# Performance work log

Hardware: AMD Instinct MI355X
Metric: run time of the kernel (lower is better)

## Reference

```python
import jax, jax.numpy as jnp
import numpy as np

DIM, HEADS, DIM_HEAD = 1024, 16, 64
DIM_INNER = HEADS * DIM_HEAD  # 1024
SCALE = DIM_HEAD ** -0.5


def _rope(t):
    # t: [b, h, n, d]; interleaved-pair RoPE (lucidrains rotary-embedding-torch default)
    d = t.shape[-1]
    n = t.shape[-2]
    inv_freq = 1.0 / (10000.0 ** (jnp.arange(0, d, 2, dtype=jnp.float32) / d))
    angles = jnp.arange(n, dtype=jnp.float32)[:, None] * inv_freq[None, :]  # [n, d/2]
    cos, sin = jnp.cos(angles), jnp.sin(angles)
    t1, t2 = t[..., 0::2], t[..., 1::2]
    r1 = t1 * cos - t2 * sin
    r2 = t1 * sin + t2 * cos
    return jnp.stack([r1, r2], axis=-1).reshape(t.shape)


def setup_inputs() -> dict:
    key = jax.random.key(0)
    ks = jax.random.split(key, 8)
    b, n = 2, 2048
    inp = {
        "x": jax.random.normal(ks[0], (b, n, DIM), dtype=jnp.float32),
        "value_residual": jax.random.normal(ks[1], (b, HEADS, n, DIM_HEAD), dtype=jnp.float32),
        "gamma": jnp.ones((DIM,), dtype=jnp.float32),
        "w_qkv": jax.random.normal(ks[2], (DIM, 3 * DIM_INNER), dtype=jnp.float32) * (DIM ** -0.5),
        "w_mix": jax.random.normal(ks[3], (DIM, HEADS), dtype=jnp.float32) * (DIM ** -0.5),
        "b_mix": jnp.zeros((HEADS,), dtype=jnp.float32),
        "w_gates": jax.random.normal(ks[4], (DIM, HEADS), dtype=jnp.float32) * (DIM ** -0.5),
        "b_gates": jnp.zeros((HEADS,), dtype=jnp.float32),
        "w_out": jax.random.normal(ks[5], (DIM_INNER, DIM), dtype=jnp.float32) * (DIM_INNER ** -0.5),
    }
    return inp


def reference(x, value_residual, gamma, w_qkv, w_mix, b_mix, w_gates, b_gates, w_out):
    b, n, _ = x.shape
    # RMSNorm (lucidrains style: F.normalize * sqrt(dim) * gamma)
    norm = jnp.sqrt(jnp.sum(x * x, axis=-1, keepdims=True))
    xn = x / jnp.maximum(norm, 1e-12) * (DIM ** 0.5) * gamma

    qkv = xn @ w_qkv  # [b, n, 3*h*d]
    qkv = qkv.reshape(b, n, 3, HEADS, DIM_HEAD)
    q, k, v = [jnp.transpose(qkv[:, :, i], (0, 2, 1, 3)) for i in range(3)]  # [b,h,n,d]
    original_values = v

    # learned value-residual lerp
    mix = jax.nn.sigmoid(xn @ w_mix + b_mix)            # [b, n, h]
    mix = jnp.transpose(mix, (0, 2, 1))[..., None]       # [b, h, n, 1]
    v = v * (1.0 - mix) + value_residual * mix

    # rotary on q, k
    q = _rope(q)
    k = _rope(k)

    scores = jnp.einsum("bhid,bhjd->bhij", q, k) * SCALE
    attn = jax.nn.softmax(scores, axis=-1)
    out = jnp.einsum("bhij,bhjd->bhid", attn, v)         # [b, h, n, d]

    gates = jax.nn.sigmoid(xn @ w_gates + b_gates)       # [b, n, h]
    out = out * jnp.transpose(gates, (0, 2, 1))[..., None]

    out = jnp.transpose(out, (0, 2, 1, 3)).reshape(b, n, DIM_INNER)
    return out @ w_out, original_values
```

## Files before the change

kernel.cpp:

```cpp
#include <hip/hip_runtime.h>
#include <hip/hip_bf16.h>
#include <math.h>

#define DIMSZ 1024
#define HEADS 16
#define DHEAD 64
#define NSEQ  2048
#define BATCH 2
#define ROWS  (BATCH*NSEQ)
#define SCALE 0.125f
#define LOG2E 1.4426950408889634f

typedef __attribute__((ext_vector_type(8))) short short8;
typedef __attribute__((ext_vector_type(4))) float floatx4;

#define MFMA16(a,b,c) __builtin_amdgcn_mfma_f32_16x16x32_bf16(a,b,c,0,0,0)

__device__ __forceinline__ void gl2lds16(const void* g, void* l) {
    __builtin_amdgcn_global_load_lds(
        (const __attribute__((address_space(1))) unsigned int*)g,
        (__attribute__((address_space(3))) unsigned int*)l, 16, 0, 0);
}

__device__ __forceinline__ unsigned short bf16r(float a) {
    unsigned u = __float_as_uint(a);
    u += 0x7fff + ((u >> 16) & 1);
    return (unsigned short)(u >> 16);
}
__device__ __forceinline__ unsigned pack_bf16(float a, float b) {
    unsigned ua = __float_as_uint(a), ub = __float_as_uint(b);
    ua += 0x7fff + ((ua >> 16) & 1);
    ub += 0x7fff + ((ub >> 16) & 1);
    return (ua >> 16) | (ub & 0xffff0000u);
}
__device__ __forceinline__ float2 bf2f(unsigned u) {
    float2 r;
    r.x = __uint_as_float(u << 16);
    r.y = __uint_as_float(u & 0xffff0000u);
    return r;
}
__device__ __forceinline__ float fexp2(float x) {
#if __has_builtin(__builtin_amdgcn_exp2f)
    return __builtin_amdgcn_exp2f(x);
#else
    return exp2f(x);
#endif
}
__device__ __forceinline__ float fsin_rev(float x) {
#if __has_builtin(__builtin_amdgcn_sinf)
    return __builtin_amdgcn_sinf(x);
#else
    return __sinf(x * 6.28318530717958647692f);
#endif
}
__device__ __forceinline__ float fcos_rev(float x) {
#if __has_builtin(__builtin_amdgcn_cosf)
    return __builtin_amdgcn_cosf(x);
#else
    return __cosf(x * 6.28318530717958647692f);
#endif
}

__global__ __launch_bounds__(256) void transpose_all_kernel(
    const float* __restrict__ w_qkv, const float* __restrict__ w_out,
    const float* __restrict__ w_mix, const float* __restrict__ w_gates,
    unsigned short* __restrict__ wqkvT, unsigned short* __restrict__ woutT,
    unsigned short* __restrict__ wmgT)
{
    __shared__ float t[32][33];
    const int tx = threadIdx.x & 31, tyy = threadIdx.x >> 5;
    const int bx = blockIdx.x;
    const int k0 = blockIdx.y * 32;
    if (bx < 128) {
        const float* src;
        unsigned short* dst;
        int N, n0;
        if (bx < 96) { src = w_qkv; dst = wqkvT; N = 3*DIMSZ; n0 = bx*32; }
        else         { src = w_out; dst = woutT; N = DIMSZ;   n0 = (bx-96)*32; }
        #pragma unroll
        for (int i = 0; i < 4; i++)
            t[tyy*4 + i][tx] = src[(size_t)(k0 + tyy*4 + i)*N + n0 + tx];
        __syncthreads();
        #pragma unroll
        for (int i = 0; i < 4; i++)
            dst[(size_t)(n0 + tyy*4 + i)*DIMSZ + k0 + tx] = bf16r(t[tx][tyy*4 + i]);
    } else {
        #pragma unroll
        for (int i = 0; i < 4; i++) {
            const int kk = k0 + tyy*4 + i;
            t[tyy*4 + i][tx] = (tx < 16) ? w_mix[kk*16 + tx]
                                         : w_gates[kk*16 + (tx - 16)];
        }
        __syncthreads();
        #pragma unroll
        for (int i = 0; i < 4; i++)
            wmgT[(size_t)(tyy*4 + i)*DIMSZ + k0 + tx] = bf16r(t[tx][tyy*4 + i]);
    }
}

__global__ __launch_bounds__(256) void rmsnorm_kernel(
    const float* __restrict__ x, const float* __restrict__ gamma,
    unsigned short* __restrict__ xnb)
{
    const int row = blockIdx.x;
    const int tid = threadIdx.x;
    __shared__ float wred[4];

    const float4 xv = ((const float4*)(x + (size_t)row * DIMSZ))[tid];
    float ss = xv.x*xv.x + xv.y*xv.y + xv.z*xv.z + xv.w*xv.w;
    #pragma unroll
    for (int off = 1; off < 64; off <<= 1) ss += __shfl_xor(ss, off);
    if ((tid & 63) == 0) wred[tid >> 6] = ss;
    __syncthreads();
    const float total = wred[0] + wred[1] + wred[2] + wred[3];
    const float inv = 32.0f / fmaxf(sqrtf(total), 1e-12f);
    const float4 gv = ((const float4*)gamma)[tid];
    uint2 pk;
    pk.x = pack_bf16(xv.x * inv * gv.x, xv.y * inv * gv.y);
    pk.y = pack_bf16(xv.z * inv * gv.z, xv.w * inv * gv.w);
    ((uint2*)(xnb + (size_t)row * DIMSZ))[tid] = pk;
}

__global__ __launch_bounds__(256) void mix_gates_mfma(
    const unsigned short* __restrict__ A, const unsigned short* __restrict__ WG,
    const float* __restrict__ b_mix, const float* __restrict__ b_gates,
    float* __restrict__ mixo, float* __restrict__ gateso)
{
    __shared__ short As[128*32];
    __shared__ short Bs[32*32];
    const int tid = threadIdx.x;
    const int wv = tid >> 6, lane = tid & 63;
    const int g = lane >> 4, c = lane & 15;
    const int bm = blockIdx.x * 128;

    floatx4 acc[2][2];
    #pragma unroll
    for (int mt = 0; mt < 2; mt++)
        #pragma unroll
        for (int nt = 0; nt < 2; nt++) acc[mt][nt] = (floatx4){0.f,0.f,0.f,0.f};

    for (int k0 = 0; k0 < DIMSZ; k0 += 32) {
        __syncthreads();
        #pragma unroll
        for (int r = 0; r < 2; r++) {
            const int ch = tid + 256*r;
            const int row = ch >> 2, cc = ch & 3;
            gl2lds16(A + (size_t)(bm + row)*DIMSZ + k0 + cc*8, (void*)(As + ch*8));
        }
        if (tid < 128)
            gl2lds16(WG + (size_t)(tid >> 2)*DIMSZ + k0 + (tid & 3)*8, (void*)(Bs + tid*8));
        __syncthreads();
        short8 af[2], bf[2];
        #pragma unroll
        for (int mt = 0; mt < 2; mt++) af[mt] = *(const short8*)(As + (wv*32 + mt*16 + c)*32 + g*8);
        #pragma unroll
        for (int nt = 0; nt < 2; nt++) bf[nt] = *(const short8*)(Bs + (nt*16 + c)*32 + g*8);
        #pragma unroll
        for (int mt = 0; mt < 2; mt++)
            #pragma unroll
            for (int nt = 0; nt < 2; nt++)
                acc[mt][nt] = MFMA16(af[mt], bf[nt], acc[mt][nt]);
    }
    const float bm_c = b_mix[c], bg_c = b_gates[c];
    #pragma unroll
    for (int mt = 0; mt < 2; mt++)
        #pragma unroll
        for (int r2 = 0; r2 < 4; r2++) {
            const int row = bm + wv*32 + mt*16 + g*4 + r2;
            const float lm = acc[mt][0][r2] + bm_c;
            const float lg = acc[mt][1][r2] + bg_c;
            mixo[(size_t)row*HEADS + c]   = 1.0f / (1.0f + fexp2(-lm * LOG2E));
            gateso[(size_t)row*HEADS + c] = 1.0f / (1.0f + fexp2(-lg * LOG2E));
        }
}

__global__ __launch_bounds__(256) void gemm_qkv_mfma(
    const unsigned short* __restrict__ A, const unsigned short* __restrict__ BT,
    unsigned short* __restrict__ qb, unsigned short* __restrict__ kb,
    float* __restrict__ vb)
{
    __shared__ short As[128*32];
    __shared__ short Bs[128*32];
    const int tid = threadIdx.x;
    const int wv = tid >> 6, lane = tid & 63;
    const int g = lane >> 4, c = lane & 15;
    const int wm = wv >> 1, wn = wv & 1;
    const int bm = blockIdx.y * 128, bn = blockIdx.x * 128;

    floatx4 acc[4][4];
    #pragma unroll
    for (int mt = 0; mt < 4; mt++)
        #pragma unroll
        for (int nt = 0; nt < 4; nt++) acc[mt][nt] = (floatx4){0.f,0.f,0.f,0.f};

    for (int k0 = 0; k0 < DIMSZ; k0 += 32) {
        __syncthreads();
        #pragma unroll
        for (int r = 0; r < 2; r++) {
            const int ch = tid + 256*r;
            const int row = ch >> 2, cc = ch & 3;
            gl2lds16(A  + (size_t)(bm + row)*DIMSZ + k0 + cc*8, (void*)(As + ch*8));
            gl2lds16(BT + (size_t)(bn + row)*DIMSZ + k0 + cc*8, (void*)(Bs + ch*8));
        }
        __syncthreads();
        short8 af[4], bf[4];
        #pragma unroll
        for (int mt = 0; mt < 4; mt++) af[mt] = *(const short8*)(As + (wm*64 + mt*16 + c)*32 + g*8);
        #pragma unroll
        for (int nt = 0; nt < 4; nt++) bf[nt] = *(const short8*)(Bs + (wn*64 + nt*16 + c)*32 + g*8);
        #pragma unroll
        for (int mt = 0; mt < 4; mt++)
            #pragma unroll
            for (int nt = 0; nt < 4; nt++)
                acc[mt][nt] = MFMA16(af[mt], bf[nt], acc[mt][nt]);
    }
    __syncthreads();
    const int i3 = bn >> 10;
    const int nb = bn - (i3 << 10);
    if (i3 < 2) {
        unsigned short* dst = (i3 == 0) ? qb : kb;
        short* wbuf = As + wv*1152;
        const int rd_row = lane >> 2, seg = lane & 3;
        #pragma unroll
        for (int mt = 0; mt < 4; mt++) {
            #pragma unroll
            for (int nt = 0; nt < 4; nt++)
                #pragma unroll
                for (int r2 = 0; r2 < 4; r2++)
                    wbuf[(g*4 + r2)*72 + nt*16 + c] = (short)bf16r(acc[mt][nt][r2]);
            __builtin_amdgcn_s_waitcnt(0xc07f);
            const uint4 v0 = *(const uint4*)&wbuf[rd_row*72 + seg*16];
            const uint4 v1 = *(const uint4*)&wbuf[rd_row*72 + seg*16 + 8];
            const int row = bm + wm*64 + mt*16 + rd_row;
            const int col = nb + wn*64 + seg*16;
            const int hh = col >> 6, dd = col & 63;
            const int bb2 = row >> 11, pos = row & 2047;
            unsigned short* dp = dst + (((size_t)(bb2*HEADS + hh)*NSEQ) + pos)*DHEAD + dd;
            *(uint4*)dp = v0;
            *(uint4*)(dp + 8) = v1;
            __builtin_amdgcn_s_waitcnt(0xc07f);
        }
    } else {
        #pragma unroll
        for (int mt = 0; mt < 4; mt++)
            #pragma unroll
            for (int nt = 0; nt < 4; nt++)
                #pragma unroll
                for (int r2 = 0; r2 < 4; r2++) {
                    const int row = bm + wm*64 + mt*16 + g*4 + r2;
                    const int col = nb + wn*64 + nt*16 + c;
                    const int hh = col >> 6, dd = col & 63;
                    const int bb2 = row >> 11, pos = row & 2047;
                    vb[(((size_t)(bb2*HEADS + hh)*NSEQ) + pos)*DHEAD + dd] = acc[mt][nt][r2];
                }
    }
}

__global__ __launch_bounds__(256) void rope_blend_kernel2(
    unsigned short* __restrict__ q, unsigned short* __restrict__ k,
    const float* __restrict__ vorig, const float* __restrict__ vres,
    const float* __restrict__ mixb, unsigned short* __restrict__ vT)
{
    __shared__ unsigned short vt[64*72];
    const int tid = threadIdx.x;
    const int bh = blockIdx.y, bb = bh >> 4, h = bh & 15;
    const int p0 = blockIdx.x * 64;
    {
        const int pr = tid >> 2, d0 = (tid & 3) * 16;
        const int pos = p0 + pr;
        const size_t base = ((size_t)bh*NSEQ + pos)*DHEAD + d0;

        uint4 qr0 = *(uint4*)(q + base), qr1 = *(uint4*)(q + base + 8);
        uint4 kr0 = *(uint4*)(k + base), kr1 = *(uint4*)(k + base + 8);
        unsigned qw[8] = {qr0.x, qr0.y, qr0.z, qr0.w, qr1.x, qr1.y, qr1.z, qr1.w};
        unsigned kw[8] = {kr0.x, kr0.y, kr0.z, kr0.w, kr1.x, kr1.y, kr1.z, kr1.w};
        const float QSC = SCALE * LOG2E;
        const float posf = (float)pos;
        #pragma unroll
        for (int j = 0; j < 8; j++) {
            const float pf = (float)((d0 >> 1) + j);
            const float rev = posf * fexp2(-pf * 0.41524101186092029f
                                           - 2.6514961294723187f);
            const float rf = rev - floorf(rev);
            const float sn = fsin_rev(rf);
            const float cs = fcos_rev(rf);
            float2 qv = bf2f(qw[j]);
            float2 kv = bf2f(kw[j]);
            const float q1 = qv.x*cs - qv.y*sn, q2 = qv.x*sn + qv.y*cs;
            const float k1 = kv.x*cs - kv.y*sn, k2 = kv.x*sn + kv.y*cs;
            qw[j] = pack_bf16(q1*QSC, q2*QSC);
            kw[j] = pack_bf16(k1, k2);
        }
        *(uint4*)(q + base)     = *(uint4*)(qw + 0);
        *(uint4*)(q + base + 8) = *(uint4*)(qw + 4);
        *(uint4*)(k + base)     = *(uint4*)(kw + 0);
        *(uint4*)(k + base + 8) = *(uint4*)(kw + 4);

        float vv[16], vr[16];
        #pragma unroll
        for (int i = 0; i < 4; i++) {
            *(float4*)(vv + i*4) = *(const float4*)(vorig + base + i*4);
            *(float4*)(vr + i*4) = *(const float4*)(vres + base + i*4);
        }
        const float mx = mixb[((size_t)(bb*NSEQ + pos))*HEADS + h];
        #pragma unroll
        for (int j = 0; j < 8; j++) {
            const float b0 = vv[2*j]*(1.f-mx)   + vr[2*j]*mx;
            const float b1 = vv[2*j+1]*(1.f-mx) + vr[2*j+1]*mx;
            vt[pr*72 + d0 + 2*j]     = bf16r(b0);
            vt[pr*72 + d0 + 2*j + 1] = bf16r(b1);
        }
    }
    __syncthreads();
    {
        const int dd = tid >> 2, c0 = (tid & 3) * 16;
        unsigned o[8];
        #pragma unroll
        for (int j = 0; j < 8; j++) {
            const unsigned a  = vt[(c0 + 2*j)*72 + dd];
            const unsigned b2 = vt[(c0 + 2*j + 1)*72 + dd];
            o[j] = a | (b2 << 16);
        }
        unsigned short* dst = vT + ((size_t)bh*DHEAD + dd)*NSEQ + p0 + c0;
        *(uint4*)(dst)     = *(uint4*)(o + 0);
        *(uint4*)(dst + 8) = *(uint4*)(o + 4);
    }
}

__global__ __launch_bounds__(256) void attn_mfma_kernel(
    const unsigned short* __restrict__ qg,
    const unsigned short* __restrict__ kg,
    const unsigned short* __restrict__ vT,
    unsigned short* __restrict__ Op0,
    unsigned short* __restrict__ Op1,
    float* __restrict__ lpart)
{
    __shared__ short Kt[64*64];
    __shared__ short Vt[64*64];
    __shared__ short Ps[4*32*64];

    const int tid = threadIdx.x;
    const int w = tid >> 6, lane = tid & 63;
    const int g = lane >> 4, c = lane & 15;
    const int byy = blockIdx.y;
    const int bh = byy >> 1, s = byy & 1;
    const int bb = bh >> 4, h = bh & 15;
    const int q0 = blockIdx.x * 128;

    short8 qf[2][2];
    #pragma unroll
    for (int mt = 0; mt < 2; mt++)
        #pragma unroll
        for (int kb = 0; kb < 2; kb++)
            qf[mt][kb] = *(const short8*)(qg + ((size_t)bh*NSEQ + q0 + w*32 + mt*16 + c)*DHEAD + kb*32 + g*8);

    floatx4 O[2][4];
    #pragma unroll
    for (int mt = 0; mt < 2; mt++)
        #pragma unroll
        for (int nt = 0; nt < 4; nt++) O[mt][nt] = (floatx4){0.f,0.f,0.f,0.f};
    float lsum[2] = {0.f, 0.f};

    short* PsW = Ps + w * 2048;
    const unsigned short* kbase = kg + (size_t)bh*NSEQ*DHEAD;
    const unsigned short* vbase = vT + (size_t)bh*DHEAD*NSEQ;

    for (int i = 0; i < 16; i++) {
        const int kt = s*16 + i;
        __syncthreads();
        #pragma unroll
        for (int r = 0; r < 2; r++) {
            const int ch = tid + 256*r;
            const int row = ch >> 3;
            const int u = (ch & 7) ^ (row & 7);
            gl2lds16(kbase + (size_t)(kt*64 + row)*DHEAD + u*8, (void*)(Kt + ch*8));
            gl2lds16(vbase + (size_t)row*NSEQ + kt*64 + u*8,   (void*)(Vt + ch*8));
        }
        __syncthreads();

        short8 kfr[4][2];
        #pragma unroll
        for (int nt = 0; nt < 4; nt++) {
            const int rowk = nt*16 + c;
            #pragma unroll
            for (int kb = 0; kb < 2; kb++)
                kfr[nt][kb] = *(const short8*)(Kt + rowk*64 + (((kb*4 + g) ^ (rowk & 7)) * 8));
        }

        #pragma unroll
        for (int mt = 0; mt < 2; mt++) {
            const int rr = mt*16 + c;
            #pragma unroll
            for (int nt = 0; nt < 4; nt++) {
                floatx4 accS = (floatx4){0.f,0.f,0.f,0.f};
                #pragma unroll
                for (int kb = 0; kb < 2; kb++)
                    accS = MFMA16(kfr[nt][kb], qf[mt][kb], accS);
                const float p0 = fexp2(accS[0]);
                const float p1 = fexp2(accS[1]);
                const float p2 = fexp2(accS[2]);
                const float p3 = fexp2(accS[3]);
                lsum[mt] += (p0 + p1) + (p2 + p3);
                uint2 pk;
                pk.x = pack_bf16(p0, p1);
                pk.y = pack_bf16(p2, p3);
                *(uint2*)(PsW + rr*64 + (((nt*2 + (g >> 1)) ^ (rr & 7)) * 8) + (g & 1)*4) = pk;
            }
        }
        __builtin_amdgcn_s_waitcnt(0xc07f);
        #pragma unroll
        for (int kb = 0; kb < 2; kb++) {
            short8 pf[2];
            #pragma unroll
            for (int mt = 0; mt < 2; mt++) {
                const int rr = mt*16 + c;
                pf[mt] = *(const short8*)(PsW + rr*64 + (((kb*4 + g) ^ (rr & 7)) * 8));
            }
            #pragma unroll
            for (int nt = 0; nt < 4; nt++) {
                const int rv = nt*16 + c;
                short8 vf = *(const short8*)(Vt + rv*64 + (((kb*4 + g) ^ (rv & 7)) * 8));
                #pragma unroll
                for (int mt = 0; mt < 2; mt++)
                    O[mt][nt] = MFMA16(pf[mt], vf, O[mt][nt]);
            }
        }
    }

    unsigned short* Op = s ? Op1 : Op0;
    #pragma unroll
    for (int mt = 0; mt < 2; mt++) {
        float l = lsum[mt];
        l += __shfl_xor(l, 16);
        l += __shfl_xor(l, 32);
        if (g == 0) {
            const int rowl = q0 + w*32 + mt*16 + c;
            lpart[((size_t)s*ROWS + bb*NSEQ + rowl)*HEADS + h] = l;
        }
        #pragma unroll
        for (int r2 = 0; r2 < 4; r2++) {
            const int rowg = q0 + w*32 + mt*16 + g*4 + r2;
            unsigned short* op = Op + ((size_t)(bb*NSEQ + rowg))*DIMSZ + h*DHEAD + c;
            #pragma unroll
            for (int nt = 0; nt < 4; nt++)
                op[nt*16] = bf16r(O[mt][nt][r2]);
        }
    }
}

__global__ __launch_bounds__(256) void attn_combine_kernel(
    const unsigned short* __restrict__ Op1, const float* __restrict__ lpart,
    const float* __restrict__ gates, unsigned short* __restrict__ attnO)
{
    const int idx = blockIdx.x * 256 + threadIdx.x;
    const int row = idx >> 7;
    const int c8 = (idx & 127) * 8;
    const int h = c8 >> 6;
    const float l0 = lpart[(size_t)row*HEADS + h];
    const float l1 = lpart[((size_t)ROWS + row)*HEADS + h];
    const float gt = gates[(size_t)row*HEADS + h];
    const float sc = gt / (l0 + l1);
    const size_t base = (size_t)row*DIMSZ + c8;
    const uint4 a = *(const uint4*)(attnO + base);
    const uint4 b = *(const uint4*)(Op1 + base);
    const unsigned aw[4] = {a.x, a.y, a.z, a.w};
    const unsigned bw[4] = {b.x, b.y, b.z, b.w};
    unsigned o[4];
    #pragma unroll
    for (int j = 0; j < 4; j++) {
        const float2 fa = bf2f(aw[j]);
        const float2 fb = bf2f(bw[j]);
        o[j] = pack_bf16((fa.x + fb.x)*sc, (fa.y + fb.y)*sc);
    }
    *(uint4*)(attnO + base) = *(uint4*)o;
}

__global__ __launch_bounds__(256) void gemm_out_mfma(
    const unsigned short* __restrict__ A, const unsigned short* __restrict__ BT,
    float* __restrict__ out0)
{
    __shared__ short As[128*32];
    __shared__ short Bs[128*32];
    const int tid = threadIdx.x;
    const int wv = tid >> 6, lane = tid & 63;
    const int g = lane >> 4, c = lane & 15;
    const int wm = wv >> 1, wn = wv & 1;
    const int bm = blockIdx.y * 128, bn = blockIdx.x * 128;

    floatx4 acc[4][4];
    #pragma unroll
    for (int mt = 0; mt < 4; mt++)
        #pragma unroll
        for (int nt = 0; nt < 4; nt++) acc[mt][nt] = (floatx4){0.f,0.f,0.f,0.f};

    for (int k0 = 0; k0 < DIMSZ; k0 += 32) {
        __syncthreads();
        #pragma unroll
        for (int r = 0; r < 2; r++) {
            const int ch = tid + 256*r;
            const int row = ch >> 2, cc = ch & 3;
            gl2lds16(A  + (size_t)(bm + row)*DIMSZ + k0 + cc*8, (void*)(As + ch*8));
            gl2lds16(BT + (size_t)(bn + row)*DIMSZ + k0 + cc*8, (void*)(Bs + ch*8));
        }
        __syncthreads();
        short8 af[4], bf[4];
        #pragma unroll
        for (int mt = 0; mt < 4; mt++) af[mt] = *(const short8*)(As + (wm*64 + mt*16 + c)*32 + g*8);
        #pragma unroll
        for (int nt = 0; nt < 4; nt++) bf[nt] = *(const short8*)(Bs + (wn*64 + nt*16 + c)*32 + g*8);
        #pragma unroll
        for (int mt = 0; mt < 4; mt++)
            #pragma unroll
            for (int nt = 0; nt < 4; nt++)
                acc[mt][nt] = MFMA16(af[mt], bf[nt], acc[mt][nt]);
    }
    #pragma unroll
    for (int mt = 0; mt < 4; mt++)
        #pragma unroll
        for (int nt = 0; nt < 4; nt++)
            #pragma unroll
            for (int r2 = 0; r2 < 4; r2++) {
                const int row = bm + wm*64 + mt*16 + g*4 + r2;
                const int col = bn + wn*64 + nt*16 + c;
                out0[(size_t)row*DIMSZ + col] = acc[mt][nt][r2];
            }
}

extern "C" void kernel_launch(void* const* d_in, const int* in_sizes, int n_in,
                              void* d_out, int out_size, void* d_ws, size_t ws_size,
                              hipStream_t stream) {
    const float* x       = (const float*)d_in[0];
    const float* vres    = (const float*)d_in[1];
    const float* gamma   = (const float*)d_in[2];
    const float* w_qkv   = (const float*)d_in[3];
    const float* w_mix   = (const float*)d_in[4];
    const float* b_mix   = (const float*)d_in[5];
    const float* w_gates = (const float*)d_in[6];
    const float* b_gates = (const float*)d_in[7];
    const float* w_out   = (const float*)d_in[8];

    float* out0 = (float*)d_out;
    float* out1 = out0 + (size_t)ROWS * DIMSZ;

    char* ws = (char*)d_ws;
    unsigned short* xnb   = (unsigned short*)(ws);
    unsigned short* wqkvT = (unsigned short*)(ws + (8u<<20));
    unsigned short* woutT = (unsigned short*)(ws + (14u<<20));
    unsigned short* qb2   = (unsigned short*)(ws + (16u<<20));
    unsigned short* kb2   = (unsigned short*)(ws + (24u<<20));
    unsigned short* vT    = (unsigned short*)(ws + (32u<<20));
    unsigned short* attnO = (unsigned short*)(ws + (40u<<20));
    float*          mixb  = (float*)(ws + (48u<<20));
    float*          gatesb= (float*)(ws + (48u<<20) + 262144);
    unsigned short* wmgT  = (unsigned short*)(ws + (49u<<20));
    unsigned short* Op1   = (unsigned short*)(ws + (50u<<20));
    float*          lpart = (float*)(ws + (58u<<20));

    transpose_all_kernel<<<dim3(129, DIMSZ/32), 256, 0, stream>>>(
        w_qkv, w_out, w_mix, w_gates, wqkvT, woutT, wmgT);

    rmsnorm_kernel<<<ROWS, 256, 0, stream>>>(x, gamma, xnb);

    mix_gates_mfma<<<ROWS/128, 256, 0, stream>>>(
        xnb, wmgT, b_mix, b_gates, mixb, gatesb);

    gemm_qkv_mfma<<<dim3(3*DIMSZ/128, ROWS/128), 256, 0, stream>>>(
        xnb, wqkvT, qb2, kb2, out1);

    rope_blend_kernel2<<<dim3(NSEQ/64, BATCH*HEADS), 256, 0, stream>>>(
        qb2, kb2, out1, vres, mixb, vT);

    attn_mfma_kernel<<<dim3(NSEQ/128, BATCH*HEADS*2), 256, 0, stream>>>(
        qb2, kb2, vT, attnO, Op1, lpart);

    attn_combine_kernel<<<ROWS*DIMSZ/8/256, 256, 0, stream>>>(
        Op1, lpart, gatesb, attnO);

    gemm_out_mfma<<<dim3(DIMSZ/128, ROWS/128), 256, 0, stream>>>(
        attnO, woutT, out0);
}
```

Measured before the change: 259.7 us.

## Merge prep kernels, fold mix/gates GEMM into QKV launch, transpose MFMA outputs

Merges the RMSNorm and weight-transpose kernels into one launch, and runs the mix/gates projection as an extra column of blocks inside the QKV GEMM grid. This cuts two kernel launches and their serialization gaps. The MFMA operands are swapped in the QKV GEMM, attention PV and output GEMM so each lane holds four consecutive output columns, which allows vectorized uint2/float4 stores and removes the LDS staging in the QKV epilogue. In attention, the softmax row sums now come from an MFMA against a ones vector over the bf16 P tiles instead of per-lane fp32 adds and shuffles. That sums the rounded bf16 probabilities, which changes numerics slightly.

```diff
diff --git a/kernel.cpp b/kernel.cpp
--- a/kernel.cpp
+++ b/kernel.cpp
@@ -61,16 +61,38 @@
 #endif
 }
 
-__global__ __launch_bounds__(256) void transpose_all_kernel(
+__global__ __launch_bounds__(256) void prep_kernel(
+    const float* __restrict__ x, const float* __restrict__ gamma,
     const float* __restrict__ w_qkv, const float* __restrict__ w_out,
     const float* __restrict__ w_mix, const float* __restrict__ w_gates,
-    unsigned short* __restrict__ wqkvT, unsigned short* __restrict__ woutT,
-    unsigned short* __restrict__ wmgT)
+    unsigned short* __restrict__ xnb, unsigned short* __restrict__ wqkvT,
+    unsigned short* __restrict__ woutT, unsigned short* __restrict__ wmgT)
 {
     __shared__ float t[32][33];
-    const int tx = threadIdx.x & 31, tyy = threadIdx.x >> 5;
-    const int bx = blockIdx.x;
-    const int k0 = blockIdx.y * 32;
+    __shared__ float wred[4];
+    const int bid = blockIdx.x;
+    const int tid = threadIdx.x;
+    if (bid < ROWS) {
+        const int row = bid;
+        const float4 xv = ((const float4*)(x + (size_t)row * DIMSZ))[tid];
+        float ss = xv.x*xv.x + xv.y*xv.y + xv.z*xv.z + xv.w*xv.w;
+        #pragma unroll
+        for (int off = 1; off < 64; off <<= 1) ss += __shfl_xor(ss, off);
+        if ((tid & 63) == 0) wred[tid >> 6] = ss;
+        __syncthreads();
+        const float total = wred[0] + wred[1] + wred[2] + wred[3];
+        const float inv = 32.0f / fmaxf(sqrtf(total), 1e-12f);
+        const float4 gv = ((const float4*)gamma)[tid];
+        uint2 pk;
+        pk.x = pack_bf16(xv.x * inv * gv.x, xv.y * inv * gv.y);
+        pk.y = pack_bf16(xv.z * inv * gv.z, xv.w * inv * gv.w);
+        ((uint2*)(xnb + (size_t)row * DIMSZ))[tid] = pk;
+        return;
+    }
+    const int tt = bid - ROWS;
+    const int bx = tt >> 5;
+    const int k0 = (tt & 31) * 32;
+    const int tx = tid & 31, tyy = tid >> 5;
     if (bx < 128) {
         const float* src;
         unsigned short* dst;
@@ -98,92 +120,62 @@
     }
 }
 
-__global__ __launch_bounds__(256) void rmsnorm_kernel(
-    const float* __restrict__ x, const float* __restrict__ gamma,
-    unsigned short* __restrict__ xnb)
-{
-    const int row = blockIdx.x;
-    const int tid = threadIdx.x;
-    __shared__ float wred[4];
-
-    const float4 xv = ((const float4*)(x + (size_t)row * DIMSZ))[tid];
-    float ss = xv.x*xv.x + xv.y*xv.y + xv.z*xv.z + xv.w*xv.w;
-    #pragma unroll
-    for (int off = 1; off < 64; off <<= 1) ss += __shfl_xor(ss, off);
-    if ((tid & 63) == 0) wred[tid >> 6] = ss;
-    __syncthreads();
-    const float total = wred[0] + wred[1] + wred[2] + wred[3];
-    const float inv = 32.0f / fmaxf(sqrtf(total), 1e-12f);
-    const float4 gv = ((const float4*)gamma)[tid];
-    uint2 pk;
-    pk.x = pack_bf16(xv.x * inv * gv.x, xv.y * inv * gv.y);
-    pk.y = pack_bf16(xv.z * inv * gv.z, xv.w * inv * gv.w);
-    ((uint2*)(xnb + (size_t)row * DIMSZ))[tid] = pk;
-}
-
-__global__ __launch_bounds__(256) void mix_gates_mfma(
-    const unsigned short* __restrict__ A, const unsigned short* __restrict__ WG,
-    const float* __restrict__ b_mix, const float* __restrict__ b_gates,
-    float* __restrict__ mixo, float* __restrict__ gateso)
-{
-    __shared__ short As[128*32];
-    __shared__ short Bs[32*32];
-    const int tid = threadIdx.x;
-    const int wv = tid >> 6, lane = tid & 63;
-    const int g = lane >> 4, c = lane & 15;
-    const int bm = blockIdx.x * 128;
-
-    floatx4 acc[2][2];
-    #pragma unroll
-    for (int mt = 0; mt < 2; mt++)
-        #pragma unroll
-        for (int nt = 0; nt < 2; nt++) acc[mt][nt] = (floatx4){0.f,0.f,0.f,0.f};
-
-    for (int k0 = 0; k0 < DIMSZ; k0 += 32) {
-        __syncthreads();
-        #pragma unroll
-        for (int r = 0; r < 2; r++) {
-            const int ch = tid + 256*r;
-            const int row = ch >> 2, cc = ch & 3;
-            gl2lds16(A + (size_t)(bm + row)*DIMSZ + k0 + cc*8, (void*)(As + ch*8));
-        }
-        if (tid < 128)
-            gl2lds16(WG + (size_t)(tid >> 2)*DIMSZ + k0 + (tid & 3)*8, (void*)(Bs + tid*8));
-        __syncthreads();
-        short8 af[2], bf[2];
-        #pragma unroll
-        for (int mt = 0; mt < 2; mt++) af[mt] = *(const short8*)(As + (wv*32 + mt*16 + c)*32 + g*8);
-        #pragma unroll
-        for (int nt = 0; nt < 2; nt++) bf[nt] = *(const short8*)(Bs + (nt*16 + c)*32 + g*8);
-        #pragma unroll
-        for (int mt = 0; mt < 2; mt++)
-            #pragma unroll
-            for (int nt = 0; nt < 2; nt++)
-                acc[mt][nt] = MFMA16(af[mt], bf[nt], acc[mt][nt]);
-    }
-    const float bm_c = b_mix[c], bg_c = b_gates[c];
-    #pragma unroll
-    for (int mt = 0; mt < 2; mt++)
-        #pragma unroll
-        for (int r2 = 0; r2 < 4; r2++) {
-            const int row = bm + wv*32 + mt*16 + g*4 + r2;
-            const float lm = acc[mt][0][r2] + bm_c;
-            const float lg = acc[mt][1][r2] + bg_c;
-            mixo[(size_t)row*HEADS + c]   = 1.0f / (1.0f + fexp2(-lm * LOG2E));
-            gateso[(size_t)row*HEADS + c] = 1.0f / (1.0f + fexp2(-lg * LOG2E));
-        }
-}
-
 __global__ __launch_bounds__(256) void gemm_qkv_mfma(
     const unsigned short* __restrict__ A, const unsigned short* __restrict__ BT,
+    const unsigned short* __restrict__ WG,
+    const float* __restrict__ b_mix, const float* __restrict__ b_gates,
     unsigned short* __restrict__ qb, unsigned short* __restrict__ kb,
-    float* __restrict__ vb)
+    float* __restrict__ vb, float* __restrict__ mixo, float* __restrict__ gateso)
 {
     __shared__ short As[128*32];
     __shared__ short Bs[128*32];
     const int tid = threadIdx.x;
     const int wv = tid >> 6, lane = tid & 63;
     const int g = lane >> 4, c = lane & 15;
+
+    if (blockIdx.x == 24) {
+        const int bm = blockIdx.y * 128;
+        floatx4 acc[2][2];
+        #pragma unroll
+        for (int mt = 0; mt < 2; mt++)
+            #pragma unroll
+            for (int nt = 0; nt < 2; nt++) acc[mt][nt] = (floatx4){0.f,0.f,0.f,0.f};
+        for (int k0 = 0; k0 < DIMSZ; k0 += 32) {
+            __syncthreads();
+            #pragma unroll
+            for (int r = 0; r < 2; r++) {
+                const int ch = tid + 256*r;
+                const int row = ch >> 2, cc = ch & 3;
+                gl2lds16(A + (size_t)(bm + row)*DIMSZ + k0 + cc*8, (void*)(As + ch*8));
+            }
+            if (tid < 128)
+                gl2lds16(WG + (size_t)(tid >> 2)*DIMSZ + k0 + (tid & 3)*8, (void*)(Bs + tid*8));
+            __syncthreads();
+            short8 af[2], bf[2];
+            #pragma unroll
+            for (int mt = 0; mt < 2; mt++) af[mt] = *(const short8*)(As + (wv*32 + mt*16 + c)*32 + g*8);
+            #pragma unroll
+            for (int nt = 0; nt < 2; nt++) bf[nt] = *(const short8*)(Bs + (nt*16 + c)*32 + g*8);
+            #pragma unroll
+            for (int mt = 0; mt < 2; mt++)
+                #pragma unroll
+                for (int nt = 0; nt < 2; nt++)
+                    acc[mt][nt] = MFMA16(af[mt], bf[nt], acc[mt][nt]);
+        }
+        const float bm_c = b_mix[c], bg_c = b_gates[c];
+        #pragma unroll
+        for (int mt = 0; mt < 2; mt++)
+            #pragma unroll
+            for (int r2 = 0; r2 < 4; r2++) {
+                const int row = bm + wv*32 + mt*16 + g*4 + r2;
+                const float lm = acc[mt][0][r2] + bm_c;
+                const float lg = acc[mt][1][r2] + bg_c;
+                mixo[(size_t)row*HEADS + c]   = 1.0f / (1.0f + fexp2(-lm * LOG2E));
+                gateso[(size_t)row*HEADS + c] = 1.0f / (1.0f + fexp2(-lg * LOG2E));
+            }
+        return;
+    }
+
     const int wm = wv >> 1, wn = wv & 1;
     const int bm = blockIdx.y * 128, bn = blockIdx.x * 128;
 
@@ -212,47 +204,41 @@
         for (int mt = 0; mt < 4; mt++)
             #pragma unroll
             for (int nt = 0; nt < 4; nt++)
-                acc[mt][nt] = MFMA16(af[mt], bf[nt], acc[mt][nt]);
-    }
-    __syncthreads();
+                acc[mt][nt] = MFMA16(bf[nt], af[mt], acc[mt][nt]);
+    }
     const int i3 = bn >> 10;
     const int nb = bn - (i3 << 10);
     if (i3 < 2) {
         unsigned short* dst = (i3 == 0) ? qb : kb;
-        short* wbuf = As + wv*1152;
-        const int rd_row = lane >> 2, seg = lane & 3;
         #pragma unroll
         for (int mt = 0; mt < 4; mt++) {
-            #pragma unroll
-            for (int nt = 0; nt < 4; nt++)
-                #pragma unroll
-                for (int r2 = 0; r2 < 4; r2++)
-                    wbuf[(g*4 + r2)*72 + nt*16 + c] = (short)bf16r(acc[mt][nt][r2]);
-            __builtin_amdgcn_s_waitcnt(0xc07f);
-            const uint4 v0 = *(const uint4*)&wbuf[rd_row*72 + seg*16];
-            const uint4 v1 = *(const uint4*)&wbuf[rd_row*72 + seg*16 + 8];
-            const int row = bm + wm*64 + mt*16 + rd_row;
-            const int col = nb + wn*64 + seg*16;
-            const int hh = col >> 6, dd = col & 63;
+            const int row = bm + wm*64 + mt*16 + c;
             const int bb2 = row >> 11, pos = row & 2047;
-            unsigned short* dp = dst + (((size_t)(bb2*HEADS + hh)*NSEQ) + pos)*DHEAD + dd;
-            *(uint4*)dp = v0;
-            *(uint4*)(dp + 8) = v1;
-            __builtin_amdgcn_s_waitcnt(0xc07f);
+            #pragma unroll
+            for (int nt = 0; nt < 4; nt++) {
+                const int col = nb + wn*64 + nt*16 + g*4;
+                const int hh = col >> 6, dd = col & 63;
+                uint2 pk;
+                pk.x = pack_bf16(acc[mt][nt][0], acc[mt][nt][1]);
+                pk.y = pack_bf16(acc[mt][nt][2], acc[mt][nt][3]);
+                *(uint2*)(dst + (((size_t)(bb2*HEADS + hh)*NSEQ) + pos)*DHEAD + dd) = pk;
+            }
         }
     } else {
         #pragma unroll
-        for (int mt = 0; mt < 4; mt++)
-            #pragma unroll
-            for (int nt = 0; nt < 4; nt++)
-                #pragma unroll
-                for (int r2 = 0; r2 < 4; r2++) {
-                    const int row = bm + wm*64 + mt*16 + g*4 + r2;
-                    const int col = nb + wn*64 + nt*16 + c;
-                    const int hh = col >> 6, dd = col & 63;
-                    const int bb2 = row >> 11, pos = row & 2047;
-                    vb[(((size_t)(bb2*HEADS + hh)*NSEQ) + pos)*DHEAD + dd] = acc[mt][nt][r2];
-                }
+        for (int mt = 0; mt < 4; mt++) {
+            const int row = bm + wm*64 + mt*16 + c;
+            const int bb2 = row >> 11, pos = row & 2047;
+            #pragma unroll
+            for (int nt = 0; nt < 4; nt++) {
+                const int col = nb + wn*64 + nt*16 + g*4;
+                const int hh = col >> 6, dd = col & 63;
+                float4 o;
+                o.x = acc[mt][nt][0]; o.y = acc[mt][nt][1];
+                o.z = acc[mt][nt][2]; o.w = acc[mt][nt][3];
+                *(float4*)(vb + (((size_t)(bb2*HEADS + hh)*NSEQ) + pos)*DHEAD + dd) = o;
+            }
+        }
     }
 }
 
@@ -354,12 +340,18 @@
         for (int kb = 0; kb < 2; kb++)
             qf[mt][kb] = *(const short8*)(qg + ((size_t)bh*NSEQ + q0 + w*32 + mt*16 + c)*DHEAD + kb*32 + g*8);
 
+    short8 ones;
+    #pragma unroll
+    for (int j = 0; j < 8; j++) ones[j] = (short)0x3f80;
+
     floatx4 O[2][4];
-    #pragma unroll
-    for (int mt = 0; mt < 2; mt++)
+    floatx4 lacc[2];
+    #pragma unroll
+    for (int mt = 0; mt < 2; mt++) {
+        lacc[mt] = (floatx4){0.f,0.f,0.f,0.f};
         #pragma unroll
         for (int nt = 0; nt < 4; nt++) O[mt][nt] = (floatx4){0.f,0.f,0.f,0.f};
-    float lsum[2] = {0.f, 0.f};
+    }
 
     short* PsW = Ps + w * 2048;
     const unsigned short* kbase = kg + (size_t)bh*NSEQ*DHEAD;
@@ -396,14 +388,9 @@
                 #pragma unroll
                 for (int kb = 0; kb < 2; kb++)
                     accS = MFMA16(kfr[nt][kb], qf[mt][kb], accS);
-                const float p0 = fexp2(accS[0]);
-                const float p1 = fexp2(accS[1]);
-                const float p2 = fexp2(accS[2]);
-                const float p3 = fexp2(accS[3]);
-                lsum[mt] += (p0 + p1) + (p2 + p3);
                 uint2 pk;
-                pk.x = pack_bf16(p0, p1);
-                pk.y = pack_bf16(p2, p3);
+                pk.x = pack_bf16(fexp2(accS[0]), fexp2(accS[1]));
+                pk.y = pack_bf16(fexp2(accS[2]), fexp2(accS[3]));
                 *(uint2*)(PsW + rr*64 + (((nt*2 + (g >> 1)) ^ (rr & 7)) * 8) + (g & 1)*4) = pk;
             }
         }
@@ -415,6 +402,7 @@
             for (int mt = 0; mt < 2; mt++) {
                 const int rr = mt*16 + c;
                 pf[mt] = *(const short8*)(PsW + rr*64 + (((kb*4 + g) ^ (rr & 7)) * 8));
+                lacc[mt] = MFMA16(ones, pf[mt], lacc[mt]);
             }
             #pragma unroll
             for (int nt = 0; nt < 4; nt++) {
@@ -422,7 +410,7 @@
                 short8 vf = *(const short8*)(Vt + rv*64 + (((kb*4 + g) ^ (rv & 7)) * 8));
                 #pragma unroll
                 for (int mt = 0; mt < 2; mt++)
-                    O[mt][nt] = MFMA16(pf[mt], vf, O[mt][nt]);
+                    O[mt][nt] = MFMA16(vf, pf[mt], O[mt][nt]);
             }
         }
     }
@@ -430,20 +418,16 @@
     unsigned short* Op = s ? Op1 : Op0;
     #pragma unroll
     for (int mt = 0; mt < 2; mt++) {
-        float l = lsum[mt];
-        l += __shfl_xor(l, 16);
-        l += __shfl_xor(l, 32);
-        if (g == 0) {
-            const int rowl = q0 + w*32 + mt*16 + c;
-            lpart[((size_t)s*ROWS + bb*NSEQ + rowl)*HEADS + h] = l;
-        }
-        #pragma unroll
-        for (int r2 = 0; r2 < 4; r2++) {
-            const int rowg = q0 + w*32 + mt*16 + g*4 + r2;
-            unsigned short* op = Op + ((size_t)(bb*NSEQ + rowg))*DIMSZ + h*DHEAD + c;
-            #pragma unroll
-            for (int nt = 0; nt < 4; nt++)
-                op[nt*16] = bf16r(O[mt][nt][r2]);
+        const int rowg = q0 + w*32 + mt*16 + c;
+        if (g == 0)
+            lpart[((size_t)s*ROWS + bb*NSEQ + rowg)*HEADS + h] = lacc[mt][0];
+        unsigned short* op = Op + ((size_t)(bb*NSEQ + rowg))*DIMSZ + h*DHEAD;
+        #pragma unroll
+        for (int nt = 0; nt < 4; nt++) {
+            uint2 pk;
+            pk.x = pack_bf16(O[mt][nt][0], O[mt][nt][1]);
+            pk.y = pack_bf16(O[mt][nt][2], O[mt][nt][3]);
+            *(uint2*)(op + nt*16 + g*4) = pk;
         }
     }
 }
@@ -512,18 +496,20 @@
         for (int mt = 0; mt < 4; mt++)
             #pragma unroll
             for (int nt = 0; nt < 4; nt++)
-                acc[mt][nt] = MFMA16(af[mt], bf[nt], acc[mt][nt]);
-    }
-    #pragma unroll
-    for (int mt = 0; mt < 4; mt++)
-        #pragma unroll
-        for (int nt = 0; nt < 4; nt++)
-            #pragma unroll
-            for (int r2 = 0; r2 < 4; r2++) {
-                const int row = bm + wm*64 + mt*16 + g*4 + r2;
-                const int col = bn + wn*64 + nt*16 + c;
-                out0[(size_t)row*DIMSZ + col] = acc[mt][nt][r2];
-            }
+                acc[mt][nt] = MFMA16(bf[nt], af[mt], acc[mt][nt]);
+    }
+    #pragma unroll
+    for (int mt = 0; mt < 4; mt++) {
+        const int row = bm + wm*64 + mt*16 + c;
+        #pragma unroll
+        for (int nt = 0; nt < 4; nt++) {
+            const int col = bn + wn*64 + nt*16 + g*4;
+            float4 o;
+            o.x = acc[mt][nt][0]; o.y = acc[mt][nt][1];
+            o.z = acc[mt][nt][2]; o.w = acc[mt][nt][3];
+            *(float4*)(out0 + (size_t)row*DIMSZ + col) = o;
+        }
+    }
 }
 
 extern "C" void kernel_launch(void* const* d_in, const int* in_sizes, int n_in,
@@ -556,16 +542,11 @@
     unsigned short* Op1   = (unsigned short*)(ws + (50u<<20));
     float*          lpart = (float*)(ws + (58u<<20));
 
-    transpose_all_kernel<<<dim3(129, DIMSZ/32), 256, 0, stream>>>(
-        w_qkv, w_out, w_mix, w_gates, wqkvT, woutT, wmgT);
-
-    rmsnorm_kernel<<<ROWS, 256, 0, stream>>>(x, gamma, xnb);
-
-    mix_gates_mfma<<<ROWS/128, 256, 0, stream>>>(
-        xnb, wmgT, b_mix, b_gates, mixb, gatesb);
-
-    gemm_qkv_mfma<<<dim3(3*DIMSZ/128, ROWS/128), 256, 0, stream>>>(
-        xnb, wqkvT, qb2, kb2, out1);
+    prep_kernel<<<ROWS + 129*32, 256, 0, stream>>>(
+        x, gamma, w_qkv, w_out, w_mix, w_gates, xnb, wqkvT, woutT, wmgT);
+
+    gemm_qkv_mfma<<<dim3(25, ROWS/128), 256, 0, stream>>>(
+        xnb, wqkvT, wmgT, b_mix, b_gates, qb2, kb2, out1, mixb, gatesb);
 
     rope_blend_kernel2<<<dim3(NSEQ/64, BATCH*HEADS), 256, 0, stream>>>(
         qb2, kb2, out1, vres, mixb, vT);
```

After: 267.0 us. 2.8% more time.
